# Kernel optimization log

Hardware: AMD Instinct MI355X
Metric: run time of the kernel (lower is better)

The kernel has to match this reference:

```python
import jax, jax.numpy as jnp
import numpy as np
import math

N_HEADS = 4


def setup_inputs() -> dict:
    key = jax.random.key(0)
    ks = jax.random.split(key, 5)
    Bs, M, T, C = 4, 190, 512, 64
    x = jax.random.normal(ks[0], (Bs, M, T, C), dtype=jnp.float32)
    s = 1.0 / math.sqrt(C)
    Wq = jax.random.normal(ks[1], (C, C), dtype=jnp.float32) * s
    Wk = jax.random.normal(ks[2], (C, C), dtype=jnp.float32) * s
    Wv = jax.random.normal(ks[3], (C, C), dtype=jnp.float32) * s
    Wp = jax.random.normal(ks[4], (C, C), dtype=jnp.float32) * s
    z = jnp.zeros((C,), dtype=jnp.float32)
    return {"x": x, "Wq": Wq, "bq": z, "Wk": Wk, "bk": z, "Wv": Wv, "bv": z, "Wp": Wp, "bp": z}


def reference(x, Wq, bq, Wk, bk, Wv, bv, Wp, bp):
    # AxialMultiAttention forward, tied=True, linear=False, dropout=0 (eval).
    Bs, M, T, C = x.shape
    N, D = N_HEADS, C // N_HEADS

    def heads(y):  # [Bs,M,T,C] -> [Bs,M,N,T,D]
        return y.reshape(Bs, M, T, N, D).transpose(0, 1, 3, 2, 4)

    q = heads(x @ Wq + bq)
    k = heads(x @ Wk + bk)
    v = heads(x @ Wv + bv)

    # tied: sum queries/keys over the axial (pair) dim M, keepdim -> size-1 axis
    q_t = q.sum(axis=1)  # [Bs,N,T,D]
    k_t = k.sum(axis=1)  # [Bs,N,T,D]
    scale = 1.0 / math.sqrt(D * M)
    weights = jax.nn.softmax(jnp.einsum('bnqd,bnkd->bnqk', q_t, k_t) * scale, axis=-1)  # [Bs,N,T,T]

    # broadcast tied weights across M when multiplying values
    att = jnp.einsum('bnqk,bmnkd->bmnqd', weights, v)  # [Bs,M,N,T,D]
    att = att.transpose(0, 1, 3, 2, 4).reshape(Bs, M, T, N * D)
    out = att @ Wp + bp  # [Bs,M,T,C]

    # a = weights.detach()[0].mean(0): weights has keepdim axis of size 1 in torch,
    # so [0] -> [1,N,T,T] and mean over dim 0 -> [N,T,T]
    a = jax.lax.stop_gradient(weights)[0]  # [N,T,T]
    return out, a
```

## Files before the change

kernel.cpp:

```cpp
#include <hip/hip_runtime.h>

typedef unsigned short ushort_t;
typedef __bf16 bf16x8 __attribute__((ext_vector_type(8)));
typedef float f32x4 __attribute__((ext_vector_type(4)));

#define DEVI __device__ __forceinline__

constexpr int BSZ = 4;
constexpr int MDIM = 190;
constexpr int TDIM = 512;
constexpr int CDIM = 64;

DEVI ushort_t f2bf(float f) {
    union { float f; unsigned int u; } v; v.f = f;
    unsigned int u = v.u;
    u += 0x7FFFu + ((u >> 16) & 1u);
    return (ushort_t)(u >> 16);
}

DEVI void gload16(ushort_t* ldsBase, const ushort_t* g) {
    __builtin_amdgcn_global_load_lds(
        (const __attribute__((address_space(1))) unsigned int*)g,
        (__attribute__((address_space(3))) unsigned int*)ldsBase, 16, 0, 0);
}

__global__ __launch_bounds__(256, 4) void k_vproj(const float* __restrict__ x,
                                                  const float* __restrict__ Wv,
                                                  const float* __restrict__ bv,
                                                  ushort_t* __restrict__ vt,
                                                  float* __restrict__ xsp) {
    __shared__ __align__(16) ushort_t xbf[64 * 72];
    __shared__ __align__(16) ushort_t WvT[64 * 72];
    __shared__ __align__(16) ushort_t vst[64 * 72];

    int tid = threadIdx.x;
    int bid = blockIdx.x;
    int mg = bid & 15;
    int tt = (bid >> 4) & 7;
    int b = bid >> 7;
    int t0 = tt * 64;
    int mbase = mg * 12;
    int cnt = (mbase + 12 <= MDIM) ? 12 : (MDIM - mbase);

    int w = tid >> 6, lane = tid & 63;
    int la = lane & 15, lb = lane >> 4;
    int r = tid >> 2, seg = tid & 3;

#pragma unroll
    for (int rep = 0; rep < 16; ++rep) {
        int j = rep * 256 + tid;
        int ci = j >> 6, co = j & 63;
        WvT[co * 72 + ci] = f2bf(Wv[j]);
    }
    float bvv[4];
#pragma unroll
    for (int cf = 0; cf < 4; ++cf) bvv[cf] = bv[16 * cf + la];

    float xacc[16];
#pragma unroll
    for (int u = 0; u < 16; ++u) xacc[u] = 0.f;

    const size_t mstride = (size_t)TDIM * CDIM;
    size_t xaddr = ((size_t)(b * MDIM + mbase) * TDIM + t0 + r) * CDIM + seg * 16;

    float4 xv[4];
#pragma unroll
    for (int u = 0; u < 4; ++u) xv[u] = *(const float4*)(x + xaddr + u * 4);

    f32x4 zz = {0.f, 0.f, 0.f, 0.f};

    for (int i = 0; i < cnt; ++i) {
#pragma unroll
        for (int u = 0; u < 4; ++u) {
            xacc[u * 4 + 0] += xv[u].x;
            xacc[u * 4 + 1] += xv[u].y;
            xacc[u * 4 + 2] += xv[u].z;
            xacc[u * 4 + 3] += xv[u].w;
            ushort4 h;
            h.x = f2bf(xv[u].x); h.y = f2bf(xv[u].y);
            h.z = f2bf(xv[u].z); h.w = f2bf(xv[u].w);
            *(ushort4*)&xbf[r * 72 + seg * 16 + u * 4] = h;
        }
        __syncthreads();

        int inext = (i + 1 < cnt) ? (i + 1) : i;
        size_t xaddr2 = xaddr + (size_t)(inext - i) * mstride;
        float4 xv2[4];
#pragma unroll
        for (int u = 0; u < 4; ++u) xv2[u] = *(const float4*)(x + xaddr2 + u * 4);

        f32x4 acc2[4];
#pragma unroll
        for (int cf = 0; cf < 4; ++cf) acc2[cf] = zz;
#pragma unroll
        for (int ks = 0; ks < 2; ++ks) {
            bf16x8 aa = *(const bf16x8*)&xbf[(w * 16 + la) * 72 + ks * 32 + lb * 8];
#pragma unroll
            for (int cf = 0; cf < 4; ++cf) {
                bf16x8 bb = *(const bf16x8*)&WvT[(16 * cf + la) * 72 + ks * 32 + lb * 8];
                acc2[cf] = __builtin_amdgcn_mfma_f32_16x16x32_bf16(aa, bb, acc2[cf], 0, 0, 0);
            }
        }
#pragma unroll
        for (int cf = 0; cf < 4; ++cf) {
            ushort4 h;
            h.x = f2bf(acc2[cf][0] + bvv[cf]);
            h.y = f2bf(acc2[cf][1] + bvv[cf]);
            h.z = f2bf(acc2[cf][2] + bvv[cf]);
            h.w = f2bf(acc2[cf][3] + bvv[cf]);
            *(ushort4*)&vst[(16 * cf + la) * 72 + w * 16 + lb * 4] = h;
        }
        __syncthreads();

        int m = mbase + i;
        size_t vbase = ((size_t)(b * MDIM + m) * CDIM + r) * TDIM + t0 + seg * 16;
        *(uint4*)(vt + vbase) = *(const uint4*)&vst[r * 72 + seg * 16];
        *(uint4*)(vt + vbase + 8) = *(const uint4*)&vst[r * 72 + seg * 16 + 8];

#pragma unroll
        for (int u = 0; u < 4; ++u) xv[u] = xv2[u];
        xaddr = xaddr2;
    }

    size_t sbase = ((size_t)(mg * 4 + b) * TDIM + t0 + r) * CDIM + seg * 16;
#pragma unroll
    for (int u = 0; u < 4; ++u) {
        float4 o;
        o.x = xacc[u * 4 + 0]; o.y = xacc[u * 4 + 1];
        o.z = xacc[u * 4 + 2]; o.w = xacc[u * 4 + 3];
        *(float4*)(xsp + sbase + u * 4) = o;
    }
}

__global__ __launch_bounds__(256) void k_xsum2(const float* __restrict__ xsp,
                                               float* __restrict__ xsum) {
    int idx = blockIdx.x * 256 + threadIdx.x;
    float s = 0.f;
#pragma unroll
    for (int p = 0; p < 16; ++p) s += xsp[(size_t)p * 131072 + idx];
    xsum[idx] = s;
}

__global__ __launch_bounds__(256) void k_weights(const float* __restrict__ xsum,
                                                 const float* __restrict__ Wq,
                                                 const float* __restrict__ bq,
                                                 const float* __restrict__ Wk,
                                                 const float* __restrict__ bk,
                                                 ushort_t* __restrict__ wbf,
                                                 float* __restrict__ a_out) {
    __shared__ __align__(16) float kt[512][20];
    __shared__ __align__(16) float qt[32][20];
    __shared__ __align__(16) float xs[64][68];
    __shared__ __align__(16) float wcol[64][16];
    __shared__ float kbias[16], qbias[16];

    int tid = threadIdx.x;
    int bid = blockIdx.x;
    int tcn = bid & 15;
    int n = (bid >> 4) & 3;
    int b = bid >> 6;
    int t0 = tcn * 32;

    for (int j = tid; j < 1024; j += 256) {
        int c = j >> 4, d = j & 15;
        wcol[c][d] = Wk[c * 64 + n * 16 + d];
    }
    if (tid < 16) kbias[tid] = 190.0f * bk[n * 16 + tid];
    if (tid >= 16 && tid < 32) qbias[tid - 16] = 190.0f * bq[n * 16 + tid - 16];
    __syncthreads();

    for (int ch = 0; ch < 8; ++ch) {
        for (int j = tid; j < 4096; j += 256) {
            int t = j >> 6, c = j & 63;
            xs[t][c] = xsum[((size_t)(b * 512) + (ch * 64 + t)) * 64 + c];
        }
        __syncthreads();
#pragma unroll
        for (int o = 0; o < 4; ++o) {
            int oi = o * 256 + tid;
            int t = oi >> 4, d = oi & 15;
            float s = 0.f;
#pragma unroll
            for (int c = 0; c < 64; ++c) s += xs[t][c] * wcol[c][d];
            kt[ch * 64 + t][d] = s + kbias[d];
        }
        __syncthreads();
    }

    for (int j = tid; j < 1024; j += 256) {
        int c = j >> 4, d = j & 15;
        wcol[c][d] = Wq[c * 64 + n * 16 + d];
    }
    for (int j = tid; j < 2048; j += 256) {
        int t = j >> 6, c = j & 63;
        xs[t][c] = xsum[((size_t)(b * 512) + (t0 + t)) * 64 + c];
    }
    __syncthreads();
#pragma unroll
    for (int o = 0; o < 2; ++o) {
        int oi = o * 256 + tid;
        int t = oi >> 4, d = oi & 15;
        float s = 0.f;
#pragma unroll
        for (int c = 0; c < 64; ++c) s += xs[t][c] * wcol[c][d];
        qt[t][d] = s + qbias[d];
    }
    __syncthreads();

    const float scale = 0.01813692f;
    int w = tid >> 6, lane = tid & 63;
    for (int rr = 0; rr < 8; ++rr) {
        int r = w * 8 + rr;
        float qreg[16];
#pragma unroll
        for (int d = 0; d < 16; ++d) qreg[d] = qt[r][d];
        float lv[8];
#pragma unroll
        for (int i = 0; i < 8; ++i) {
            int k = lane + 64 * i;
            const float* kr = &kt[k][0];
            float s = 0.f;
#pragma unroll
            for (int d = 0; d < 16; ++d) s += qreg[d] * kr[d];
            lv[i] = s * scale;
        }
        float mx = lv[0];
#pragma unroll
        for (int i = 1; i < 8; ++i) mx = fmaxf(mx, lv[i]);
#pragma unroll
        for (int off = 32; off >= 1; off >>= 1) mx = fmaxf(mx, __shfl_xor(mx, off));
        float se = 0.f;
#pragma unroll
        for (int i = 0; i < 8; ++i) { lv[i] = __expf(lv[i] - mx); se += lv[i]; }
#pragma unroll
        for (int off = 32; off >= 1; off >>= 1) se += __shfl_xor(se, off);
        float inv = 1.0f / se;

        size_t wbase = ((size_t)((b * 4 + n) * 512 + (t0 + r))) * 512;
        size_t abase = ((size_t)(n * 512 + (t0 + r))) * 512;
#pragma unroll
        for (int i = 0; i < 8; ++i) {
            float wv = lv[i] * inv;
            wbf[wbase + lane + 64 * i] = f2bf(wv);
            if (b == 0) a_out[abase + lane + 64 * i] = wv;
        }
    }
}

__global__ __launch_bounds__(256, 3) void k_att(const ushort_t* __restrict__ wbf,
                                                const ushort_t* __restrict__ vt,
                                                const float* __restrict__ Wp,
                                                const float* __restrict__ bp,
                                                float* __restrict__ out) {
    __shared__ __align__(16) ushort_t lds[24576];

    int tid = threadIdx.x;
    int bid0 = blockIdx.x;
    int bid = (bid0 & 7) * 96 + (bid0 >> 3);
    int ttile = bid & 7;
    int mt = (bid >> 3) % 24;
    int b = bid / 192;
    int t0 = ttile * 64;

    int w = tid >> 6, lane = tid & 63;
    int la = lane & 15, lb = lane >> 4;

    unsigned wbase0[2]; int wldso[2];
#pragma unroll
    for (int cw = 0; cw < 2; ++cw) {
        int ci = w * 2 + cw;
        int u = ci * 64 + lane;
        int r = u >> 2;
        int s = (u & 3) ^ ((r >> 1) & 3);
        int nn = r >> 6, trel = r & 63;
        wbase0[cw] = (unsigned)(((b * 4 + nn) * 512 + t0 + trel) * 512 + s * 8);
        wldso[cw] = ci * 512;
    }
    unsigned vbase0[4]; int vldso[4];
#pragma unroll
    for (int cv = 0; cv < 4; ++cv) {
        int cj = w * 4 + cv;
        int u = cj * 64 + lane;
        int r = u >> 2;
        int s = (u & 3) ^ ((r >> 1) & 3);
        int mrel = r >> 5, crel = r & 31;
        int mg = mt * 8 + mrel; if (mg > 189) mg = 189;
        vbase0[cv] = (unsigned)(((b * 190 + mg) * 64 + crel) * 512 + s * 8);
        vldso[cv] = 4096 + cj * 512;
    }

    int offA[2][4], offB[2][2];
#pragma unroll
    for (int nn = 0; nn < 2; ++nn) {
#pragma unroll
        for (int q = 0; q < 4; ++q) {
            int row = nn * 64 + 16 * q + la;
            offA[nn][q] = row * 32 + (lb ^ ((row >> 1) & 3)) * 8;
        }
#pragma unroll
        for (int pp = 0; pp < 2; ++pp) {
            int row = (w * 2 + pp) * 32 + nn * 16 + la;
            offB[pp][nn] = 4096 + row * 32 + (lb ^ ((row >> 1) & 3)) * 8;
        }
    }

    f32x4 zz = {0.f, 0.f, 0.f, 0.f};
    f32x4 acc[2][4][4];
#pragma unroll
    for (int p = 0; p < 2; ++p)
#pragma unroll
        for (int n = 0; n < 4; ++n)
#pragma unroll
            for (int q = 0; q < 4; ++q) acc[p][n][q] = zz;

#define STAGE(KC, NP, PAR) do {                                                   \
    int phW = (NP) * 524288 + (KC) * 32;                                          \
    int phV = (NP) * 16384 + (KC) * 32;                                           \
    ushort_t* bufb = lds + (PAR) * 12288;                                         \
    gload16(bufb + wldso[0], wbf + wbase0[0] + phW);                              \
    gload16(bufb + wldso[1], wbf + wbase0[1] + phW);                              \
    gload16(bufb + vldso[0], vt + vbase0[0] + phV);                               \
    gload16(bufb + vldso[1], vt + vbase0[1] + phV);                               \
    gload16(bufb + vldso[2], vt + vbase0[2] + phV);                               \
    gload16(bufb + vldso[3], vt + vbase0[3] + phV);                               \
} while (0)

#define COMPUTE(NP, PAR) do {                                                     \
    const ushort_t* bufc = lds + (PAR) * 12288;                                   \
    __builtin_amdgcn_s_setprio(1);                                                \
    _Pragma("unroll")                                                             \
    for (int nn = 0; nn < 2; ++nn) {                                              \
        bf16x8 bb0 = *(const bf16x8*)(bufc + offB[0][nn]);                        \
        bf16x8 bb1 = *(const bf16x8*)(bufc + offB[1][nn]);                        \
        _Pragma("unroll")                                                         \
        for (int q = 0; q < 4; ++q) {                                             \
            bf16x8 aa = *(const bf16x8*)(bufc + offA[nn][q]);                     \
            acc[0][(NP)*2+nn][q] = __builtin_amdgcn_mfma_f32_16x16x32_bf16(aa, bb0, acc[0][(NP)*2+nn][q], 0, 0, 0); \
            acc[1][(NP)*2+nn][q] = __builtin_amdgcn_mfma_f32_16x16x32_bf16(aa, bb1, acc[1][(NP)*2+nn][q], 0, 0, 0); \
        }                                                                         \
    }                                                                             \
    __builtin_amdgcn_s_setprio(0);                                                \
} while (0)

#define VMW6 asm volatile("s_waitcnt vmcnt(6)" ::: "memory")
#define VMW0 asm volatile("s_waitcnt vmcnt(0)" ::: "memory")

    STAGE(0, 0, 0);
    STAGE(0, 1, 1);

    for (int kc = 0; kc < 15; ++kc) {
        VMW6;
        __builtin_amdgcn_s_barrier();
        COMPUTE(0, 0);
        __builtin_amdgcn_s_barrier();
        STAGE(kc + 1, 0, 0);
        VMW6;
        __builtin_amdgcn_s_barrier();
        COMPUTE(1, 1);
        __builtin_amdgcn_s_barrier();
        STAGE(kc + 1, 1, 1);
    }
    VMW6;
    __builtin_amdgcn_s_barrier();
    COMPUTE(0, 0);
    VMW0;
    __builtin_amdgcn_s_barrier();
    COMPUTE(1, 1);
    __syncthreads();
#undef STAGE
#undef COMPUTE
#undef VMW6
#undef VMW0

#pragma unroll
    for (int rep = 0; rep < 16; ++rep) {
        int j = rep * 256 + tid;
        int ci2 = j >> 6, co = j & 63;
        lds[18432 + co * 72 + ci2] = f2bf(Wp[j]);
    }
    float bpv[4];
#pragma unroll
    for (int cf = 0; cf < 4; ++cf) bpv[cf] = bp[16 * cf + la];

    for (int p = 0; p < 2; ++p) {
        int m = mt * 8 + w * 2 + p;
#pragma unroll
        for (int n = 0; n < 4; ++n)
#pragma unroll
            for (int q = 0; q < 4; ++q)
#pragma unroll
                for (int r = 0; r < 4; ++r)
                    lds[(w * 64 + 16 * q + lb * 4 + r) * 72 + 16 * n + la] = f2bf(acc[p][n][q][r]);
        __syncthreads();

        f32x4 acc2[4][4];
#pragma unroll
        for (int q = 0; q < 4; ++q)
#pragma unroll
            for (int cf = 0; cf < 4; ++cf) acc2[q][cf] = zz;
#pragma unroll
        for (int ks = 0; ks < 2; ++ks) {
            bf16x8 wb[4];
#pragma unroll
            for (int cf = 0; cf < 4; ++cf)
                wb[cf] = *(const bf16x8*)(lds + 18432 + (16 * cf + la) * 72 + ks * 32 + lb * 8);
#pragma unroll
            for (int q = 0; q < 4; ++q) {
                bf16x8 aa = *(const bf16x8*)(lds + (w * 64 + 16 * q + la) * 72 + ks * 32 + lb * 8);
#pragma unroll
                for (int cf = 0; cf < 4; ++cf)
                    acc2[q][cf] = __builtin_amdgcn_mfma_f32_16x16x32_bf16(aa, wb[cf], acc2[q][cf], 0, 0, 0);
            }
        }
        if (m < 190) {
            size_t obase = ((size_t)(b * 190 + m) * 512 + t0) * 64;
#pragma unroll
            for (int q = 0; q < 4; ++q)
#pragma unroll
                for (int r = 0; r < 4; ++r) {
                    int t = 16 * q + lb * 4 + r;
#pragma unroll
                    for (int cf = 0; cf < 4; ++cf)
                        out[obase + (size_t)t * 64 + 16 * cf + la] = acc2[q][cf][r] + bpv[cf];
                }
        }
        __syncthreads();
    }
}

extern "C" void kernel_launch(void* const* d_in, const int* in_sizes, int n_in,
                              void* d_out, int out_size, void* d_ws, size_t ws_size,
                              hipStream_t stream) {
    const float* x  = (const float*)d_in[0];
    const float* Wq = (const float*)d_in[1];
    const float* bq = (const float*)d_in[2];
    const float* Wk = (const float*)d_in[3];
    const float* bk = (const float*)d_in[4];
    const float* Wv = (const float*)d_in[5];
    const float* bv = (const float*)d_in[6];
    const float* Wp = (const float*)d_in[7];
    const float* bp = (const float*)d_in[8];

    float* out = (float*)d_out;
    float* a_out = out + (size_t)BSZ * MDIM * TDIM * CDIM;

    float* xsp = out;

    float* xsum = (float*)d_ws;
    ushort_t* wbf = (ushort_t*)((char*)d_ws + 524288);
    ushort_t* vtb = (ushort_t*)((char*)d_ws + 524288 + 8388608);

    k_vproj<<<512, 256, 0, stream>>>(x, Wv, bv, vtb, xsp);
    k_xsum2<<<512, 256, 0, stream>>>(xsp, xsum);
    k_weights<<<256, 256, 0, stream>>>(xsum, Wq, bq, Wk, bk, wbf, a_out);
    k_att<<<768, 256, 0, stream>>>(wbf, vtb, Wp, bp, out);
}
```

Baseline: 143.9 us.

## Rewrite attention-value kernel to per-head waves with direct register loads and 32x32 MFMA

```diff
diff --git a/kernel.cpp b/kernel.cpp
--- a/kernel.cpp
+++ b/kernel.cpp
@@ -3,6 +3,7 @@
 typedef unsigned short ushort_t;
 typedef __bf16 bf16x8 __attribute__((ext_vector_type(8)));
 typedef float f32x4 __attribute__((ext_vector_type(4)));
+typedef float f32x16 __attribute__((ext_vector_type(16)));
 
 #define DEVI __device__ __forceinline__
 
@@ -16,12 +17,6 @@
     unsigned int u = v.u;
     u += 0x7FFFu + ((u >> 16) & 1u);
     return (ushort_t)(u >> 16);
-}
-
-DEVI void gload16(ushort_t* ldsBase, const ushort_t* g) {
-    __builtin_amdgcn_global_load_lds(
-        (const __attribute__((address_space(1))) unsigned int*)g,
-        (__attribute__((address_space(3))) unsigned int*)ldsBase, 16, 0, 0);
 }
 
 __global__ __launch_bounds__(256, 4) void k_vproj(const float* __restrict__ x,
@@ -247,12 +242,13 @@
     }
 }
 
-__global__ __launch_bounds__(256, 3) void k_att(const ushort_t* __restrict__ wbf,
+__global__ __launch_bounds__(256, 2) void k_att(const ushort_t* __restrict__ wbf,
                                                 const ushort_t* __restrict__ vt,
                                                 const float* __restrict__ Wp,
                                                 const float* __restrict__ bp,
                                                 float* __restrict__ out) {
-    __shared__ __align__(16) ushort_t lds[24576];
+    __shared__ __align__(16) ushort_t attS[4 * 64 * 68];
+    __shared__ __align__(16) ushort_t WpT[64 * 68];
 
     int tid = threadIdx.x;
     int bid0 = blockIdx.x;
@@ -263,168 +259,127 @@
     int t0 = ttile * 64;
 
     int w = tid >> 6, lane = tid & 63;
-    int la = lane & 15, lb = lane >> 4;
-
-    unsigned wbase0[2]; int wldso[2];
-#pragma unroll
-    for (int cw = 0; cw < 2; ++cw) {
-        int ci = w * 2 + cw;
-        int u = ci * 64 + lane;
-        int r = u >> 2;
-        int s = (u & 3) ^ ((r >> 1) & 3);
-        int nn = r >> 6, trel = r & 63;
-        wbase0[cw] = (unsigned)(((b * 4 + nn) * 512 + t0 + trel) * 512 + s * 8);
-        wldso[cw] = ci * 512;
-    }
-    unsigned vbase0[4]; int vldso[4];
-#pragma unroll
-    for (int cv = 0; cv < 4; ++cv) {
-        int cj = w * 4 + cv;
-        int u = cj * 64 + lane;
-        int r = u >> 2;
-        int s = (u & 3) ^ ((r >> 1) & 3);
-        int mrel = r >> 5, crel = r & 31;
+    int l31 = lane & 31, lhi = lane >> 5;
+    int n = w;
+
+#pragma unroll
+    for (int rep = 0; rep < 16; ++rep) {
+        int j = rep * 256 + tid;
+        int ci = j >> 6, co = j & 63;
+        WpT[co * 68 + ci] = f2bf(Wp[j]);
+    }
+
+    unsigned wbase[2];
+#pragma unroll
+    for (int q = 0; q < 2; ++q)
+        wbase[q] = (unsigned)(((b * 4 + n) * 512 + t0 + q * 32 + l31) * 512 + lhi * 8);
+    unsigned vbase[4];
+#pragma unroll
+    for (int j = 0; j < 4; ++j) {
+        int col = j * 32 + l31;
+        int mrel = col >> 4, d = col & 15;
         int mg = mt * 8 + mrel; if (mg > 189) mg = 189;
-        vbase0[cv] = (unsigned)(((b * 190 + mg) * 64 + crel) * 512 + s * 8);
-        vldso[cv] = 4096 + cj * 512;
-    }
-
-    int offA[2][4], offB[2][2];
-#pragma unroll
-    for (int nn = 0; nn < 2; ++nn) {
-#pragma unroll
-        for (int q = 0; q < 4; ++q) {
-            int row = nn * 64 + 16 * q + la;
-            offA[nn][q] = row * 32 + (lb ^ ((row >> 1) & 3)) * 8;
-        }
-#pragma unroll
-        for (int pp = 0; pp < 2; ++pp) {
-            int row = (w * 2 + pp) * 32 + nn * 16 + la;
-            offB[pp][nn] = 4096 + row * 32 + (lb ^ ((row >> 1) & 3)) * 8;
-        }
-    }
-
-    f32x4 zz = {0.f, 0.f, 0.f, 0.f};
-    f32x4 acc[2][4][4];
-#pragma unroll
-    for (int p = 0; p < 2; ++p)
-#pragma unroll
-        for (int n = 0; n < 4; ++n)
-#pragma unroll
-            for (int q = 0; q < 4; ++q) acc[p][n][q] = zz;
-
-#define STAGE(KC, NP, PAR) do {                                                   \
-    int phW = (NP) * 524288 + (KC) * 32;                                          \
-    int phV = (NP) * 16384 + (KC) * 32;                                           \
-    ushort_t* bufb = lds + (PAR) * 12288;                                         \
-    gload16(bufb + wldso[0], wbf + wbase0[0] + phW);                              \
-    gload16(bufb + wldso[1], wbf + wbase0[1] + phW);                              \
-    gload16(bufb + vldso[0], vt + vbase0[0] + phV);                               \
-    gload16(bufb + vldso[1], vt + vbase0[1] + phV);                               \
-    gload16(bufb + vldso[2], vt + vbase0[2] + phV);                               \
-    gload16(bufb + vldso[3], vt + vbase0[3] + phV);                               \
+        vbase[j] = (unsigned)(((b * 190 + mg) * 64 + n * 16 + d) * 512 + lhi * 8);
+    }
+
+    f32x16 acc[2][4];
+#pragma unroll
+    for (int q = 0; q < 2; ++q)
+#pragma unroll
+        for (int j = 0; j < 4; ++j) acc[q][j] = (f32x16)(0.f);
+
+    bf16x8 Ae[2][2], Be[2][4], Ao[2][2], Bo[2][4];
+
+#define LOADC(A_, B_, KC) do {                                                    \
+    int ko = (KC) * 32;                                                           \
+    _Pragma("unroll")                                                             \
+    for (int kk = 0; kk < 2; ++kk) {                                              \
+        _Pragma("unroll")                                                         \
+        for (int q = 0; q < 2; ++q)                                               \
+            A_[kk][q] = *(const bf16x8*)(wbf + wbase[q] + ko + kk * 16);          \
+        _Pragma("unroll")                                                         \
+        for (int j = 0; j < 4; ++j)                                               \
+            B_[kk][j] = *(const bf16x8*)(vt + vbase[j] + ko + kk * 16);           \
+    }                                                                             \
 } while (0)
 
-#define COMPUTE(NP, PAR) do {                                                     \
-    const ushort_t* bufc = lds + (PAR) * 12288;                                   \
+#define COMPC(A_, B_) do {                                                        \
     __builtin_amdgcn_s_setprio(1);                                                \
     _Pragma("unroll")                                                             \
-    for (int nn = 0; nn < 2; ++nn) {                                              \
-        bf16x8 bb0 = *(const bf16x8*)(bufc + offB[0][nn]);                        \
-        bf16x8 bb1 = *(const bf16x8*)(bufc + offB[1][nn]);                        \
+    for (int kk = 0; kk < 2; ++kk)                                                \
         _Pragma("unroll")                                                         \
-        for (int q = 0; q < 4; ++q) {                                             \
-            bf16x8 aa = *(const bf16x8*)(bufc + offA[nn][q]);                     \
-            acc[0][(NP)*2+nn][q] = __builtin_amdgcn_mfma_f32_16x16x32_bf16(aa, bb0, acc[0][(NP)*2+nn][q], 0, 0, 0); \
-            acc[1][(NP)*2+nn][q] = __builtin_amdgcn_mfma_f32_16x16x32_bf16(aa, bb1, acc[1][(NP)*2+nn][q], 0, 0, 0); \
-        }                                                                         \
-    }                                                                             \
+        for (int q = 0; q < 2; ++q)                                               \
+            _Pragma("unroll")                                                     \
+            for (int j = 0; j < 4; ++j)                                           \
+                acc[q][j] = __builtin_amdgcn_mfma_f32_32x32x16_bf16(A_[kk][q], B_[kk][j], acc[q][j], 0, 0, 0); \
     __builtin_amdgcn_s_setprio(0);                                                \
 } while (0)
 
-#define VMW6 asm volatile("s_waitcnt vmcnt(6)" ::: "memory")
-#define VMW0 asm volatile("s_waitcnt vmcnt(0)" ::: "memory")
-
-    STAGE(0, 0, 0);
-    STAGE(0, 1, 1);
-
-    for (int kc = 0; kc < 15; ++kc) {
-        VMW6;
-        __builtin_amdgcn_s_barrier();
-        COMPUTE(0, 0);
-        __builtin_amdgcn_s_barrier();
-        STAGE(kc + 1, 0, 0);
-        VMW6;
-        __builtin_amdgcn_s_barrier();
-        COMPUTE(1, 1);
-        __builtin_amdgcn_s_barrier();
-        STAGE(kc + 1, 1, 1);
-    }
-    VMW6;
-    __builtin_amdgcn_s_barrier();
-    COMPUTE(0, 0);
-    VMW0;
-    __builtin_amdgcn_s_barrier();
-    COMPUTE(1, 1);
-    __syncthreads();
-#undef STAGE
-#undef COMPUTE
-#undef VMW6
-#undef VMW0
-
-#pragma unroll
-    for (int rep = 0; rep < 16; ++rep) {
-        int j = rep * 256 + tid;
-        int ci2 = j >> 6, co = j & 63;
-        lds[18432 + co * 72 + ci2] = f2bf(Wp[j]);
-    }
-    float bpv[4];
-#pragma unroll
-    for (int cf = 0; cf < 4; ++cf) bpv[cf] = bp[16 * cf + la];
-
-    for (int p = 0; p < 2; ++p) {
-        int m = mt * 8 + w * 2 + p;
-#pragma unroll
-        for (int n = 0; n < 4; ++n)
-#pragma unroll
-            for (int q = 0; q < 4; ++q)
-#pragma unroll
-                for (int r = 0; r < 4; ++r)
-                    lds[(w * 64 + 16 * q + lb * 4 + r) * 72 + 16 * n + la] = f2bf(acc[p][n][q][r]);
-        __syncthreads();
-
-        f32x4 acc2[4][4];
-#pragma unroll
-        for (int q = 0; q < 4; ++q)
-#pragma unroll
-            for (int cf = 0; cf < 4; ++cf) acc2[q][cf] = zz;
-#pragma unroll
-        for (int ks = 0; ks < 2; ++ks) {
-            bf16x8 wb[4];
-#pragma unroll
-            for (int cf = 0; cf < 4; ++cf)
-                wb[cf] = *(const bf16x8*)(lds + 18432 + (16 * cf + la) * 72 + ks * 32 + lb * 8);
-#pragma unroll
-            for (int q = 0; q < 4; ++q) {
-                bf16x8 aa = *(const bf16x8*)(lds + (w * 64 + 16 * q + la) * 72 + ks * 32 + lb * 8);
-#pragma unroll
-                for (int cf = 0; cf < 4; ++cf)
-                    acc2[q][cf] = __builtin_amdgcn_mfma_f32_16x16x32_bf16(aa, wb[cf], acc2[q][cf], 0, 0, 0);
+    LOADC(Ae, Be, 0);
+    LOADC(Ao, Bo, 1);
+#pragma unroll
+    for (int kc = 0; kc < 16; kc += 2) {
+        COMPC(Ae, Be);
+        if (kc + 2 < 16) LOADC(Ae, Be, kc + 2);
+        COMPC(Ao, Bo);
+        if (kc + 3 < 16) LOADC(Ao, Bo, kc + 3);
+    }
+#undef LOADC
+#undef COMPC
+
+    float bpv[2];
+#pragma unroll
+    for (int cf = 0; cf < 2; ++cf) bpv[cf] = bp[cf * 32 + l31];
+
+#pragma unroll
+    for (int h = 0; h < 2; ++h) {
+        __syncthreads();
+#pragma unroll
+        for (int q = 0; q < 2; ++q)
+#pragma unroll
+            for (int jj = 0; jj < 2; ++jj) {
+                f32x16 a = acc[q][h * 2 + jj];
+                int mloc = jj * 2 + (l31 >> 4);
+                int d = l31 & 15;
+#pragma unroll
+                for (int r = 0; r < 16; ++r) {
+                    int t = q * 32 + (r & 3) + 8 * (r >> 2) + 4 * lhi;
+                    attS[(mloc * 64 + t) * 68 + w * 16 + d] = f2bf(a[r]);
+                }
             }
-        }
+        __syncthreads();
+
+        f32x16 acc2[2][2];
+#pragma unroll
+        for (int q = 0; q < 2; ++q)
+#pragma unroll
+            for (int cf = 0; cf < 2; ++cf) acc2[q][cf] = (f32x16)(0.f);
+#pragma unroll
+        for (int kk = 0; kk < 4; ++kk) {
+#pragma unroll
+            for (int q = 0; q < 2; ++q) {
+                bf16x8 aa = *(const bf16x8*)(attS + (w * 64 + q * 32 + l31) * 68 + kk * 16 + lhi * 8);
+#pragma unroll
+                for (int cf = 0; cf < 2; ++cf) {
+                    bf16x8 bbf = *(const bf16x8*)(WpT + (cf * 32 + l31) * 68 + kk * 16 + lhi * 8);
+                    acc2[q][cf] = __builtin_amdgcn_mfma_f32_32x32x16_bf16(aa, bbf, acc2[q][cf], 0, 0, 0);
+                }
+            }
+        }
+        int m = mt * 8 + h * 4 + w;
         if (m < 190) {
             size_t obase = ((size_t)(b * 190 + m) * 512 + t0) * 64;
 #pragma unroll
-            for (int q = 0; q < 4; ++q)
-#pragma unroll
-                for (int r = 0; r < 4; ++r) {
-                    int t = 16 * q + lb * 4 + r;
-#pragma unroll
-                    for (int cf = 0; cf < 4; ++cf)
-                        out[obase + (size_t)t * 64 + 16 * cf + la] = acc2[q][cf][r] + bpv[cf];
-                }
-        }
-        __syncthreads();
+            for (int q = 0; q < 2; ++q)
+#pragma unroll
+                for (int cf = 0; cf < 2; ++cf)
+#pragma unroll
+                    for (int r = 0; r < 16; ++r) {
+                        int t = q * 32 + (r & 3) + 8 * (r >> 2) + 4 * lhi;
+                        int c = cf * 32 + l31;
+                        out[obase + (size_t)t * 64 + c] = acc2[q][cf][r] + bpv[cf];
+                    }
+        }
     }
 }
 
```

After: 149.9 us. 1.04x slower.
